# Performance work log

Hardware: AMD Instinct MI355X
Metric: run time of the kernel (lower is better)

The kernel has to match this reference:

```python
import jax, jax.numpy as jnp
import numpy as np

N = 16384   # flat token count
D = 256     # d_model
M = 64      # median_size (attention in_features / hidden_features)
OUT = 1     # output_size


def setup_inputs() -> dict:
    key = jax.random.key(0)
    ks = jax.random.split(key, 12)
    sD = 1.0 / np.sqrt(D)
    sM = 1.0 / np.sqrt(M)
    rn = lambda k, shape, s: (jax.random.normal(k, shape, jnp.float32) * s)
    return {
        "x":    rn(ks[0], (N, D), 1.0),
        "W1":   rn(ks[1], (D, M), sD), "b1": jnp.zeros((M,), jnp.float32),
        # 3 stacked attention blocks
        "Wq":   rn(ks[2], (3, M, M), sM), "bq": jnp.zeros((3, M), jnp.float32),
        "Wk":   rn(ks[3], (3, M, M), sM), "bk": jnp.zeros((3, M), jnp.float32),
        "Wv":   rn(ks[4], (3, M, M), sM), "bv": jnp.zeros((3, M), jnp.float32),
        "Wf1":  rn(ks[5], (3, M, M), sM), "bf1": jnp.zeros((3, M), jnp.float32),
        "Wf2":  rn(ks[6], (3, M, M), sM), "bf2": jnp.zeros((3, M), jnp.float32),
        "ln_g": jnp.ones((3, M), jnp.float32), "ln_b": jnp.zeros((3, M), jnp.float32),
        "Wout": rn(ks[7], (M, OUT), sM), "bout": jnp.zeros((OUT,), jnp.float32),
    }


def leaky(x, slope):
    return jnp.where(x >= 0, x, slope * x)


def layer_norm(x, g, b, eps=1e-5):
    mu = jnp.mean(x, axis=-1, keepdims=True)
    var = jnp.mean((x - mu) ** 2, axis=-1, keepdims=True)
    return (x - mu) * jax.lax.rsqrt(var + eps) * g + b


def attn_block(x, Wq, bq, Wk, bk, Wv, bv, Wf1, bf1, Wf2, bf2):
    # per-token outer-product attention: attn[n] = softmax(q[n] k[n]^T) over last dim
    q = x @ Wq + bq            # [N, M]
    k = x @ Wk + bk
    v = x @ Wv + bv
    a = jax.nn.softmax(q[:, :, None] * k[:, None, :], axis=-1)   # [N, M, M]
    y = jnp.einsum('nij,nj->ni', a, v) + x                       # residual add (x += x0)
    h = leaky(y @ Wf1 + bf1, 0.01)                               # LeakyReLU(0.01)
    h = h @ Wf2 + bf2
    return h + y                                                 # pred=False residual


def reference(x, W1, b1, Wq, bq, Wk, bk, Wv, bv, Wf1, bf1, Wf2, bf2, ln_g, ln_b, Wout, bout):
    h = x @ W1 + b1                 # Linear_1
    res = leaky(h, 0.1)             # x1 = LeakyReLU(0.1)(h)
    cur = h                         # transformer_1 is applied to pre-activation h
    for t in range(3):
        a = attn_block(cur, Wq[t], bq[t], Wk[t], bk[t], Wv[t], bv[t],
                       Wf1[t], bf1[t], Wf2[t], bf2[t])
        a = layer_norm(a, ln_g[t], ln_b[t])
        res = a + res               # x2 = LN(...) + x1, etc.
        cur = res
    out = leaky(res @ Wout + bout, 0.1).reshape(-1, OUT)
    return (out, out, out, out, out)
```

## Files before the change

kernel.cpp:

```cpp
#include <hip/hip_runtime.h>

#define NTOK 16384
#define TB 16

typedef float f32x4_t __attribute__((ext_vector_type(4)));
typedef short s16x8_t __attribute__((ext_vector_type(8)));
typedef short s16x4_t __attribute__((ext_vector_type(4)));

__device__ __forceinline__ unsigned short f2bf(float f) {
    unsigned int x = __float_as_uint(f);
    x += 0x7fffu + ((x >> 16) & 1u);
    return (unsigned short)(x >> 16);
}
__device__ __forceinline__ float fexp2(float x) {
#if __has_builtin(__builtin_amdgcn_exp2f)
    return __builtin_amdgcn_exp2f(x);
#else
    return exp2f(x);
#endif
}
__device__ __forceinline__ float frcp(float x) {
#if __has_builtin(__builtin_amdgcn_rcpf)
    return __builtin_amdgcn_rcpf(x);
#else
    return 1.0f / x;
#endif
}
__device__ __forceinline__ float frsq(float x) {
#if __has_builtin(__builtin_amdgcn_rsqf)
    return __builtin_amdgcn_rsqf(x);
#else
    return rsqrtf(x);
#endif
}

__global__ __launch_bounds__(256, 4)
void tf3_kernel(const float* __restrict__ x,
                const float* __restrict__ W1, const float* __restrict__ b1,
                const float* __restrict__ Wq, const float* __restrict__ bq,
                const float* __restrict__ Wk, const float* __restrict__ bk,
                const float* __restrict__ Wv, const float* __restrict__ bv,
                const float* __restrict__ Wf1, const float* __restrict__ bf1,
                const float* __restrict__ Wf2, const float* __restrict__ bf2,
                const float* __restrict__ lng, const float* __restrict__ lnb,
                const float* __restrict__ Wout, const float* __restrict__ bout,
                float* __restrict__ out)
{
    __shared__ __align__(16) unsigned short w3_lds[3 * 64 * 64];
    __shared__ __align__(16) unsigned short a_lds[TB * 64];
    __shared__ __align__(16) float q_lds[TB * 64];
    __shared__ __align__(16) float ky_lds[TB * 68];
    __shared__ __align__(16) float v_lds[TB * 64];

    const int tid = threadIdx.x;
    const int wv  = tid >> 6;
    const int l   = tid & 63;
    const int n0  = blockIdx.x * TB;

    const int lr  = l & 15;
    const int q4  = l >> 4;
    const int pcol = wv * 16;
    const int c    = pcol + lr;

    const int g  = q4;
    const int e  = lr;
    const int tg = wv * 4 + g;

    float res_reg[4], cur_reg[4];

    auto loadW = [&](const float* __restrict__ Wg, int slot, int cc) {
        s16x8_t pk;
        #pragma unroll
        for (int i = 0; i < 8; ++i)
            pk[i] = (short)f2bf(Wg[(cc * 8 + i) * 64 + l]);
        *reinterpret_cast<s16x8_t*>(&w3_lds[slot * 4096 + l * 64 + ((cc ^ (l & 7)) * 8)]) = pk;
    };
    auto mm16 = [&](const unsigned short* __restrict__ bbase) -> f32x4_t {
        f32x4_t acc = {0.f, 0.f, 0.f, 0.f};
        #pragma unroll
        for (int kh = 0; kh < 2; ++kh) {
            const int ck = kh * 4 + q4;
            const s16x8_t af = *reinterpret_cast<const s16x8_t*>(&a_lds[lr * 64 + ((ck ^ (lr & 7)) * 8)]);
            const s16x8_t bf = *reinterpret_cast<const s16x8_t*>(&bbase[c * 64 + ((ck ^ (c & 7)) * 8)]);
            acc = __builtin_amdgcn_mfma_f32_16x16x32_bf16(af, bf, acc, 0, 0, 0);
        }
        return acc;
    };

    f32x4_t acch = {0.f, 0.f, 0.f, 0.f};
    for (int kc = 0; kc < 4; ++kc) {
        __syncthreads();
        {
            const int r  = tid >> 4;
            const int c4 = (tid & 15) * 4;
            const float4 u = *reinterpret_cast<const float4*>(x + (size_t)(n0 + r) * 256 + kc * 64 + c4);
            s16x4_t pk;
            pk[0] = (short)f2bf(u.x); pk[1] = (short)f2bf(u.y);
            pk[2] = (short)f2bf(u.z); pk[3] = (short)f2bf(u.w);
            const int cc = c4 >> 3, e0 = c4 & 7;
            *reinterpret_cast<s16x4_t*>(&a_lds[r * 64 + ((cc ^ (r & 7)) * 8) + e0]) = pk;
        }
        loadW(W1 + kc * 4096, 0, wv * 2 + 0);
        loadW(W1 + kc * 4096, 0, wv * 2 + 1);
        __syncthreads();
        #pragma unroll
        for (int kh = 0; kh < 2; ++kh) {
            const int ck = kh * 4 + q4;
            const s16x8_t af = *reinterpret_cast<const s16x8_t*>(&a_lds[lr * 64 + ((ck ^ (lr & 7)) * 8)]);
            const s16x8_t bf = *reinterpret_cast<const s16x8_t*>(&w3_lds[c * 64 + ((ck ^ (c & 7)) * 8)]);
            acch = __builtin_amdgcn_mfma_f32_16x16x32_bf16(af, bf, acch, 0, 0, 0);
        }
    }
    {
        const float b1v = b1[c];
        #pragma unroll
        for (int rg = 0; rg < 4; ++rg)
            q_lds[(q4 * 4 + rg) * 64 + c] = acch[rg] + b1v;
    }
    __syncthreads();
    #pragma unroll
    for (int tt = 0; tt < 4; ++tt) {
        const int t = wv * 4 + tt;
        const float h = q_lds[t * 64 + l];
        cur_reg[tt] = h;
        res_reg[tt] = h >= 0.f ? h : 0.1f * h;
        a_lds[t * 64 + (((l >> 3) ^ (t & 7)) * 8) + (l & 7)] = f2bf(h);
    }

    for (int st = 0; st < 3; ++st) {
        const float* Wq_s  = Wq  + st * 4096;
        const float* Wk_s  = Wk  + st * 4096;
        const float* Wv_s  = Wv  + st * 4096;
        const float* Wf1_s = Wf1 + st * 4096;
        const float* Wf2_s = Wf2 + st * 4096;

        #pragma unroll
        for (int i = 0; i < 6; ++i) {
            const int u = wv * 6 + i;
            const int m = u >> 3;
            loadW(m == 0 ? Wq_s : (m == 1 ? Wk_s : Wv_s), m, u & 7);
        }
        __syncthreads();

        {
            f32x4_t aq = mm16(&w3_lds[0]);
            f32x4_t ak = mm16(&w3_lds[4096]);
            f32x4_t av = mm16(&w3_lds[8192]);
            const float bqv = bq[st * 64 + c];
            const float bkv = bk[st * 64 + c];
            const float bvv = bv[st * 64 + c];
            #pragma unroll
            for (int rg = 0; rg < 4; ++rg) {
                const int tr = q4 * 4 + rg;
                q_lds[tr * 64 + c]  = aq[rg] + bqv;
                ky_lds[tr * 68 + c] = ak[rg] + bkv;
                v_lds[tr * 64 + c]  = av[rg] + bvv;
            }
        }
        __syncthreads();

        #pragma unroll
        for (int i = 0; i < 4; ++i) {
            const int u = wv * 4 + i;
            loadW((u >> 3) == 0 ? Wf1_s : Wf2_s, u >> 3, u & 7);
        }
        float kmx, kmn;
        {
            const float4 kv = *reinterpret_cast<const float4*>(&ky_lds[tg * 68 + e * 4]);
            kmx = fmaxf(fmaxf(kv.x, kv.y), fmaxf(kv.z, kv.w));
            kmn = fminf(fminf(kv.x, kv.y), fminf(kv.z, kv.w));
            #pragma unroll
            for (int m = 1; m < 16; m <<= 1) {
                kmx = fmaxf(kmx, __shfl_xor(kmx, m, 64));
                kmn = fminf(kmn, __shfl_xor(kmn, m, 64));
            }
        }
        float kmax_t[4], kmin_t[4];
        #pragma unroll
        for (int tt = 0; tt < 4; ++tt) {
            kmax_t[tt] = __shfl(kmx, tt * 16, 64);
            kmin_t[tt] = __shfl(kmn, tt * 16, 64);
        }
        #pragma unroll
        for (int tt = 0; tt < 4; ++tt) {
            const int t = wv * 4 + tt;
            const float qs = q_lds[t * 64 + l] * 1.44269504088896340736f;
            const float m2 = fmaxf(qs * kmax_t[tt], qs * kmin_t[tt]);
            float s0 = 0.f, s1 = 0.f, p0 = 0.f, p1 = 0.f;
            #pragma unroll
            for (int j = 0; j < 64; j += 4) {
                const float4 kj = *reinterpret_cast<const float4*>(&ky_lds[t * 68 + j]);
                const float4 vj = *reinterpret_cast<const float4*>(&v_lds[t * 64 + j]);
                const float e0 = fexp2(fmaf(qs, kj.x, -m2));
                const float e1 = fexp2(fmaf(qs, kj.y, -m2));
                const float e2 = fexp2(fmaf(qs, kj.z, -m2));
                const float e3 = fexp2(fmaf(qs, kj.w, -m2));
                s0 += e0 + e2; s1 += e1 + e3;
                p0 = fmaf(e0, vj.x, p0); p1 = fmaf(e1, vj.y, p1);
                p0 = fmaf(e2, vj.z, p0); p1 = fmaf(e3, vj.w, p1);
            }
            const float y = (p0 + p1) * frcp(s0 + s1) + cur_reg[tt];
            ky_lds[t * 68 + l] = y;
        }
        __syncthreads();

        {
            f32x4_t acc = {0.f, 0.f, 0.f, 0.f};
            #pragma unroll
            for (int kh = 0; kh < 2; ++kh) {
                const float* yp = &ky_lds[lr * 68 + kh * 32 + q4 * 8];
                const float4 y0 = *reinterpret_cast<const float4*>(yp);
                const float4 y1 = *reinterpret_cast<const float4*>(yp + 4);
                s16x8_t af;
                af[0] = (short)f2bf(y0.x); af[1] = (short)f2bf(y0.y);
                af[2] = (short)f2bf(y0.z); af[3] = (short)f2bf(y0.w);
                af[4] = (short)f2bf(y1.x); af[5] = (short)f2bf(y1.y);
                af[6] = (short)f2bf(y1.z); af[7] = (short)f2bf(y1.w);
                const int ck = kh * 4 + q4;
                const s16x8_t bf = *reinterpret_cast<const s16x8_t*>(&w3_lds[c * 64 + ((ck ^ (c & 7)) * 8)]);
                acc = __builtin_amdgcn_mfma_f32_16x16x32_bf16(af, bf, acc, 0, 0, 0);
            }
            const float bfv = bf1[st * 64 + c];
            #pragma unroll
            for (int rg = 0; rg < 4; ++rg) {
                const int tr = q4 * 4 + rg;
                float h = acc[rg] + bfv;
                h = h >= 0.f ? h : 0.01f * h;
                a_lds[tr * 64 + (((c >> 3) ^ (tr & 7)) * 8) + (c & 7)] = f2bf(h);
            }
        }
        __syncthreads();

        {
            f32x4_t acc = mm16(&w3_lds[4096]);
            const float bfv = bf2[st * 64 + c];
            #pragma unroll
            for (int rg = 0; rg < 4; ++rg) {
                const int tr = q4 * 4 + rg;
                ky_lds[tr * 68 + c] += acc[rg] + bfv;
            }
        }
        __syncthreads();

        float s_sum, vsum;
        float4 av4;
        {
            av4 = *reinterpret_cast<const float4*>(&ky_lds[tg * 68 + e * 4]);
            s_sum = av4.x + av4.y + av4.z + av4.w;
            #pragma unroll
            for (int m = 1; m < 16; m <<= 1) s_sum += __shfl_xor(s_sum, m, 64);
            const float mug = s_sum * 0.015625f;
            const float d0 = av4.x - mug, d1 = av4.y - mug, d2 = av4.z - mug, d3 = av4.w - mug;
            vsum = d0 * d0 + d1 * d1 + d2 * d2 + d3 * d3;
            #pragma unroll
            for (int m = 1; m < 16; m <<= 1) vsum += __shfl_xor(vsum, m, 64);
            s_sum = mug;
        }
        const float lngv = lng[st * 64 + l];
        const float lnbv = lnb[st * 64 + l];
        #pragma unroll
        for (int tt = 0; tt < 4; ++tt) {
            const int t = wv * 4 + tt;
            const float mu = __shfl(s_sum, tt * 16, 64);
            const float vv = __shfl(vsum, tt * 16, 64);
            const float rs = frsq(vv * 0.015625f + 1e-5f);
            const float a  = ky_lds[t * 68 + l];
            const float an = (a - mu) * rs * lngv + lnbv;
            const float rnew = res_reg[tt] + an;
            res_reg[tt] = rnew;
            cur_reg[tt] = rnew;
            a_lds[t * 64 + (((l >> 3) ^ (t & 7)) * 8) + (l & 7)] = f2bf(rnew);
        }
    }

    const float wo = Wout[l];
    const float bo = bout[0];
    #pragma unroll
    for (int tt = 0; tt < 4; ++tt)
        q_lds[(wv * 4 + tt) * 64 + l] = res_reg[tt] * wo;
    {
        const float4 pv = *reinterpret_cast<const float4*>(&q_lds[tg * 64 + e * 4]);
        float p = pv.x + pv.y + pv.z + pv.w;
        #pragma unroll
        for (int m = 1; m < 16; m <<= 1) p += __shfl_xor(p, m, 64);
        if (e == 0) {
            float o = p + bo;
            o = o >= 0.f ? o : 0.1f * o;
            #pragma unroll
            for (int c5 = 0; c5 < 5; ++c5)
                out[(size_t)c5 * NTOK + n0 + tg] = o;
        }
    }
}

extern "C" void kernel_launch(void* const* d_in, const int* in_sizes, int n_in,
                              void* d_out, int out_size, void* d_ws, size_t ws_size,
                              hipStream_t stream) {
    const float* x    = (const float*)d_in[0];
    const float* W1   = (const float*)d_in[1];
    const float* b1   = (const float*)d_in[2];
    const float* Wq   = (const float*)d_in[3];
    const float* bq   = (const float*)d_in[4];
    const float* Wk   = (const float*)d_in[5];
    const float* bk   = (const float*)d_in[6];
    const float* Wv   = (const float*)d_in[7];
    const float* bv   = (const float*)d_in[8];
    const float* Wf1  = (const float*)d_in[9];
    const float* bf1  = (const float*)d_in[10];
    const float* Wf2  = (const float*)d_in[11];
    const float* bf2  = (const float*)d_in[12];
    const float* lngp = (const float*)d_in[13];
    const float* lnbp = (const float*)d_in[14];
    const float* Wout = (const float*)d_in[15];
    const float* bout = (const float*)d_in[16];
    float* outp = (float*)d_out;

    dim3 grid(NTOK / TB);
    dim3 block(256);
    hipLaunchKernelGGL(tf3_kernel, grid, block, 0, stream,
                       x, W1, b1, Wq, bq, Wk, bk, Wv, bv,
                       Wf1, bf1, Wf2, bf2, lngp, lnbp, Wout, bout, outp);
}
```

Measured before the change: 58.29 us.

## Pre-convert weights to bf16 once and read MFMA B-operands from global memory

```diff
diff --git a/kernel.cpp b/kernel.cpp
--- a/kernel.cpp
+++ b/kernel.cpp
@@ -1,11 +1,10 @@
 #include <hip/hip_runtime.h>
 
 #define NTOK 16384
-#define TB 16
+#define TB 8
 
 typedef float f32x4_t __attribute__((ext_vector_type(4)));
 typedef short s16x8_t __attribute__((ext_vector_type(8)));
-typedef short s16x4_t __attribute__((ext_vector_type(4)));
 
 __device__ __forceinline__ unsigned short f2bf(float f) {
     unsigned int x = __float_as_uint(f);
@@ -34,23 +33,42 @@
 #endif
 }
 
-__global__ __launch_bounds__(256, 4)
+__global__ __launch_bounds__(256)
+void prep_kernel(const float* __restrict__ W1,
+                 const float* __restrict__ Wq, const float* __restrict__ Wk,
+                 const float* __restrict__ Wv, const float* __restrict__ Wf1,
+                 const float* __restrict__ Wf2, unsigned short* __restrict__ wsb)
+{
+    const int i = blockIdx.x * 256 + threadIdx.x;
+    if (i < 16384) {
+        const int m = i >> 8, k = i & 255;
+        wsb[i] = f2bf(W1[k * 64 + m]);
+    } else if (i < 77824) {
+        const int u  = i - 16384;
+        const int mm = u >> 12;
+        const int st = mm / 5, q = mm % 5;
+        const int r  = u & 4095;
+        const int m  = r >> 6, k = r & 63;
+        const float* src = q == 0 ? Wq : q == 1 ? Wk : q == 2 ? Wv : q == 3 ? Wf1 : Wf2;
+        wsb[i] = f2bf(src[st * 4096 + k * 64 + m]);
+    }
+}
+
+__global__ __launch_bounds__(256, 8)
 void tf3_kernel(const float* __restrict__ x,
-                const float* __restrict__ W1, const float* __restrict__ b1,
-                const float* __restrict__ Wq, const float* __restrict__ bq,
-                const float* __restrict__ Wk, const float* __restrict__ bk,
-                const float* __restrict__ Wv, const float* __restrict__ bv,
-                const float* __restrict__ Wf1, const float* __restrict__ bf1,
-                const float* __restrict__ Wf2, const float* __restrict__ bf2,
+                const float* __restrict__ b1,
+                const float* __restrict__ bq, const float* __restrict__ bk,
+                const float* __restrict__ bv,
+                const float* __restrict__ bf1, const float* __restrict__ bf2,
                 const float* __restrict__ lng, const float* __restrict__ lnb,
                 const float* __restrict__ Wout, const float* __restrict__ bout,
+                const unsigned short* __restrict__ wsb,
                 float* __restrict__ out)
 {
-    __shared__ __align__(16) unsigned short w3_lds[3 * 64 * 64];
-    __shared__ __align__(16) unsigned short a_lds[TB * 64];
-    __shared__ __align__(16) float q_lds[TB * 64];
-    __shared__ __align__(16) float ky_lds[TB * 68];
-    __shared__ __align__(16) float v_lds[TB * 64];
+    __shared__ __align__(16) unsigned short a_lds[16 * 64];
+    __shared__ __align__(16) float q_lds[16 * 68];
+    __shared__ __align__(16) float ky_lds[16 * 68];
+    __shared__ __align__(16) float v_lds[16 * 68];
 
     const int tid = threadIdx.x;
     const int wv  = tid >> 6;
@@ -59,145 +77,113 @@
 
     const int lr  = l & 15;
     const int q4  = l >> 4;
-    const int pcol = wv * 16;
-    const int c    = pcol + lr;
-
-    const int g  = q4;
-    const int e  = lr;
-    const int tg = wv * 4 + g;
-
-    float res_reg[4], cur_reg[4];
-
-    auto loadW = [&](const float* __restrict__ Wg, int slot, int cc) {
-        s16x8_t pk;
+    const int c   = wv * 16 + lr;
+
+    const int hh = l >> 5;
+    const int e2 = l & 31;
+    const int th = wv * 2 + hh;
+
+    float res_reg[2], cur_reg[2];
+
+    {
+        const float* xrow = x + (size_t)min(n0 + lr, NTOK - 1) * 256;
+        f32x4_t acch = {0.f, 0.f, 0.f, 0.f};
         #pragma unroll
-        for (int i = 0; i < 8; ++i)
-            pk[i] = (short)f2bf(Wg[(cc * 8 + i) * 64 + l]);
-        *reinterpret_cast<s16x8_t*>(&w3_lds[slot * 4096 + l * 64 + ((cc ^ (l & 7)) * 8)]) = pk;
-    };
-    auto mm16 = [&](const unsigned short* __restrict__ bbase) -> f32x4_t {
-        f32x4_t acc = {0.f, 0.f, 0.f, 0.f};
-        #pragma unroll
-        for (int kh = 0; kh < 2; ++kh) {
-            const int ck = kh * 4 + q4;
-            const s16x8_t af = *reinterpret_cast<const s16x8_t*>(&a_lds[lr * 64 + ((ck ^ (lr & 7)) * 8)]);
-            const s16x8_t bf = *reinterpret_cast<const s16x8_t*>(&bbase[c * 64 + ((ck ^ (c & 7)) * 8)]);
-            acc = __builtin_amdgcn_mfma_f32_16x16x32_bf16(af, bf, acc, 0, 0, 0);
-        }
-        return acc;
-    };
-
-    f32x4_t acch = {0.f, 0.f, 0.f, 0.f};
-    for (int kc = 0; kc < 4; ++kc) {
-        __syncthreads();
-        {
-            const int r  = tid >> 4;
-            const int c4 = (tid & 15) * 4;
-            const float4 u = *reinterpret_cast<const float4*>(x + (size_t)(n0 + r) * 256 + kc * 64 + c4);
-            s16x4_t pk;
-            pk[0] = (short)f2bf(u.x); pk[1] = (short)f2bf(u.y);
-            pk[2] = (short)f2bf(u.z); pk[3] = (short)f2bf(u.w);
-            const int cc = c4 >> 3, e0 = c4 & 7;
-            *reinterpret_cast<s16x4_t*>(&a_lds[r * 64 + ((cc ^ (r & 7)) * 8) + e0]) = pk;
-        }
-        loadW(W1 + kc * 4096, 0, wv * 2 + 0);
-        loadW(W1 + kc * 4096, 0, wv * 2 + 1);
-        __syncthreads();
-        #pragma unroll
-        for (int kh = 0; kh < 2; ++kh) {
-            const int ck = kh * 4 + q4;
-            const s16x8_t af = *reinterpret_cast<const s16x8_t*>(&a_lds[lr * 64 + ((ck ^ (lr & 7)) * 8)]);
-            const s16x8_t bf = *reinterpret_cast<const s16x8_t*>(&w3_lds[c * 64 + ((ck ^ (c & 7)) * 8)]);
+        for (int s5 = 0; s5 < 8; ++s5) {
+            const int k0 = s5 * 32 + q4 * 8;
+            const float4 u0 = *reinterpret_cast<const float4*>(xrow + k0);
+            const float4 u1 = *reinterpret_cast<const float4*>(xrow + k0 + 4);
+            s16x8_t af;
+            af[0] = (short)f2bf(u0.x); af[1] = (short)f2bf(u0.y);
+            af[2] = (short)f2bf(u0.z); af[3] = (short)f2bf(u0.w);
+            af[4] = (short)f2bf(u1.x); af[5] = (short)f2bf(u1.y);
+            af[6] = (short)f2bf(u1.z); af[7] = (short)f2bf(u1.w);
+            const s16x8_t bf = *reinterpret_cast<const s16x8_t*>(&wsb[c * 256 + k0]);
             acch = __builtin_amdgcn_mfma_f32_16x16x32_bf16(af, bf, acch, 0, 0, 0);
         }
-    }
-    {
-        const float b1v = b1[c];
+        const float bb = b1[c];
         #pragma unroll
         for (int rg = 0; rg < 4; ++rg)
-            q_lds[(q4 * 4 + rg) * 64 + c] = acch[rg] + b1v;
+            q_lds[(q4 * 4 + rg) * 68 + c] = acch[rg] + bb;
     }
     __syncthreads();
     #pragma unroll
-    for (int tt = 0; tt < 4; ++tt) {
-        const int t = wv * 4 + tt;
-        const float h = q_lds[t * 64 + l];
+    for (int tt = 0; tt < 2; ++tt) {
+        const int t = wv * 2 + tt;
+        const float h = q_lds[t * 68 + l];
         cur_reg[tt] = h;
         res_reg[tt] = h >= 0.f ? h : 0.1f * h;
         a_lds[t * 64 + (((l >> 3) ^ (t & 7)) * 8) + (l & 7)] = f2bf(h);
     }
 
     for (int st = 0; st < 3; ++st) {
-        const float* Wq_s  = Wq  + st * 4096;
-        const float* Wk_s  = Wk  + st * 4096;
-        const float* Wv_s  = Wv  + st * 4096;
-        const float* Wf1_s = Wf1 + st * 4096;
-        const float* Wf2_s = Wf2 + st * 4096;
-
-        #pragma unroll
-        for (int i = 0; i < 6; ++i) {
-            const int u = wv * 6 + i;
-            const int m = u >> 3;
-            loadW(m == 0 ? Wq_s : (m == 1 ? Wk_s : Wv_s), m, u & 7);
-        }
-        __syncthreads();
-
-        {
-            f32x4_t aq = mm16(&w3_lds[0]);
-            f32x4_t ak = mm16(&w3_lds[4096]);
-            f32x4_t av = mm16(&w3_lds[8192]);
-            const float bqv = bq[st * 64 + c];
-            const float bkv = bk[st * 64 + c];
-            const float bvv = bv[st * 64 + c];
-            #pragma unroll
-            for (int rg = 0; rg < 4; ++rg) {
-                const int tr = q4 * 4 + rg;
-                q_lds[tr * 64 + c]  = aq[rg] + bqv;
-                ky_lds[tr * 68 + c] = ak[rg] + bkv;
-                v_lds[tr * 64 + c]  = av[rg] + bvv;
-            }
-        }
-        __syncthreads();
-
-        #pragma unroll
-        for (int i = 0; i < 4; ++i) {
-            const int u = wv * 4 + i;
-            loadW((u >> 3) == 0 ? Wf1_s : Wf2_s, u >> 3, u & 7);
-        }
-        float kmx, kmn;
-        {
-            const float4 kv = *reinterpret_cast<const float4*>(&ky_lds[tg * 68 + e * 4]);
-            kmx = fmaxf(fmaxf(kv.x, kv.y), fmaxf(kv.z, kv.w));
-            kmn = fminf(fminf(kv.x, kv.y), fminf(kv.z, kv.w));
-            #pragma unroll
-            for (int m = 1; m < 16; m <<= 1) {
+        const unsigned short* WS = wsb + 16384 + st * 5 * 4096;
+
+        __syncthreads();
+        const s16x8_t af0 = *reinterpret_cast<const s16x8_t*>(&a_lds[lr * 64 + ((q4       ^ (lr & 7)) * 8)]);
+        const s16x8_t af1 = *reinterpret_cast<const s16x8_t*>(&a_lds[lr * 64 + (((4 + q4) ^ (lr & 7)) * 8)]);
+        {
+            const s16x8_t b0 = *reinterpret_cast<const s16x8_t*>(&WS[c * 64 + q4 * 8]);
+            const s16x8_t b1f = *reinterpret_cast<const s16x8_t*>(&WS[c * 64 + 32 + q4 * 8]);
+            f32x4_t acc = __builtin_amdgcn_mfma_f32_16x16x32_bf16(af0, b0, (f32x4_t){0.f,0.f,0.f,0.f}, 0, 0, 0);
+            acc = __builtin_amdgcn_mfma_f32_16x16x32_bf16(af1, b1f, acc, 0, 0, 0);
+            const float bb = bq[st * 64 + c];
+            #pragma unroll
+            for (int rg = 0; rg < 4; ++rg) q_lds[(q4 * 4 + rg) * 68 + c] = acc[rg] + bb;
+        }
+        {
+            const s16x8_t b0 = *reinterpret_cast<const s16x8_t*>(&WS[4096 + c * 64 + q4 * 8]);
+            const s16x8_t b1f = *reinterpret_cast<const s16x8_t*>(&WS[4096 + c * 64 + 32 + q4 * 8]);
+            f32x4_t acc = __builtin_amdgcn_mfma_f32_16x16x32_bf16(af0, b0, (f32x4_t){0.f,0.f,0.f,0.f}, 0, 0, 0);
+            acc = __builtin_amdgcn_mfma_f32_16x16x32_bf16(af1, b1f, acc, 0, 0, 0);
+            const float bb = bk[st * 64 + c];
+            #pragma unroll
+            for (int rg = 0; rg < 4; ++rg) ky_lds[(q4 * 4 + rg) * 68 + c] = acc[rg] + bb;
+        }
+        {
+            const s16x8_t b0 = *reinterpret_cast<const s16x8_t*>(&WS[8192 + c * 64 + q4 * 8]);
+            const s16x8_t b1f = *reinterpret_cast<const s16x8_t*>(&WS[8192 + c * 64 + 32 + q4 * 8]);
+            f32x4_t acc = __builtin_amdgcn_mfma_f32_16x16x32_bf16(af0, b0, (f32x4_t){0.f,0.f,0.f,0.f}, 0, 0, 0);
+            acc = __builtin_amdgcn_mfma_f32_16x16x32_bf16(af1, b1f, acc, 0, 0, 0);
+            const float bb = bv[st * 64 + c];
+            #pragma unroll
+            for (int rg = 0; rg < 4; ++rg) v_lds[(q4 * 4 + rg) * 68 + c] = acc[rg] + bb;
+        }
+        __syncthreads();
+
+        float kmax_t[2], kmin_t[2];
+        {
+            const float2 kv = *reinterpret_cast<const float2*>(&ky_lds[th * 68 + e2 * 2]);
+            float kmx = fmaxf(kv.x, kv.y);
+            float kmn = fminf(kv.x, kv.y);
+            #pragma unroll
+            for (int m = 1; m < 32; m <<= 1) {
                 kmx = fmaxf(kmx, __shfl_xor(kmx, m, 64));
                 kmn = fminf(kmn, __shfl_xor(kmn, m, 64));
             }
-        }
-        float kmax_t[4], kmin_t[4];
+            #pragma unroll
+            for (int tt = 0; tt < 2; ++tt) {
+                kmax_t[tt] = __shfl(kmx, tt * 32, 64);
+                kmin_t[tt] = __shfl(kmn, tt * 32, 64);
+            }
+        }
         #pragma unroll
-        for (int tt = 0; tt < 4; ++tt) {
-            kmax_t[tt] = __shfl(kmx, tt * 16, 64);
-            kmin_t[tt] = __shfl(kmn, tt * 16, 64);
-        }
-        #pragma unroll
-        for (int tt = 0; tt < 4; ++tt) {
-            const int t = wv * 4 + tt;
-            const float qs = q_lds[t * 64 + l] * 1.44269504088896340736f;
+        for (int tt = 0; tt < 2; ++tt) {
+            const int t = wv * 2 + tt;
+            const float qs = q_lds[t * 68 + l] * 1.44269504088896340736f;
             const float m2 = fmaxf(qs * kmax_t[tt], qs * kmin_t[tt]);
             float s0 = 0.f, s1 = 0.f, p0 = 0.f, p1 = 0.f;
             #pragma unroll
             for (int j = 0; j < 64; j += 4) {
                 const float4 kj = *reinterpret_cast<const float4*>(&ky_lds[t * 68 + j]);
-                const float4 vj = *reinterpret_cast<const float4*>(&v_lds[t * 64 + j]);
+                const float4 vj = *reinterpret_cast<const float4*>(&v_lds[t * 68 + j]);
                 const float e0 = fexp2(fmaf(qs, kj.x, -m2));
                 const float e1 = fexp2(fmaf(qs, kj.y, -m2));
-                const float e2 = fexp2(fmaf(qs, kj.z, -m2));
+                const float e2v = fexp2(fmaf(qs, kj.z, -m2));
                 const float e3 = fexp2(fmaf(qs, kj.w, -m2));
-                s0 += e0 + e2; s1 += e1 + e3;
+                s0 += e0 + e2v; s1 += e1 + e3;
                 p0 = fmaf(e0, vj.x, p0); p1 = fmaf(e1, vj.y, p1);
-                p0 = fmaf(e2, vj.z, p0); p1 = fmaf(e3, vj.w, p1);
+                p0 = fmaf(e2v, vj.z, p0); p1 = fmaf(e3, vj.w, p1);
             }
             const float y = (p0 + p1) * frcp(s0 + s1) + cur_reg[tt];
             ky_lds[t * 68 + l] = y;
@@ -216,15 +202,14 @@
                 af[2] = (short)f2bf(y0.z); af[3] = (short)f2bf(y0.w);
                 af[4] = (short)f2bf(y1.x); af[5] = (short)f2bf(y1.y);
                 af[6] = (short)f2bf(y1.z); af[7] = (short)f2bf(y1.w);
-                const int ck = kh * 4 + q4;
-                const s16x8_t bf = *reinterpret_cast<const s16x8_t*>(&w3_lds[c * 64 + ((ck ^ (c & 7)) * 8)]);
+                const s16x8_t bf = *reinterpret_cast<const s16x8_t*>(&WS[3 * 4096 + c * 64 + kh * 32 + q4 * 8]);
                 acc = __builtin_amdgcn_mfma_f32_16x16x32_bf16(af, bf, acc, 0, 0, 0);
             }
-            const float bfv = bf1[st * 64 + c];
+            const float bb = bf1[st * 64 + c];
             #pragma unroll
             for (int rg = 0; rg < 4; ++rg) {
                 const int tr = q4 * 4 + rg;
-                float h = acc[rg] + bfv;
+                float h = acc[rg] + bb;
                 h = h >= 0.f ? h : 0.01f * h;
                 a_lds[tr * 64 + (((c >> 3) ^ (tr & 7)) * 8) + (c & 7)] = f2bf(h);
             }
@@ -232,63 +217,65 @@
         __syncthreads();
 
         {
-            f32x4_t acc = mm16(&w3_lds[4096]);
-            const float bfv = bf2[st * 64 + c];
+            const s16x8_t ag0 = *reinterpret_cast<const s16x8_t*>(&a_lds[lr * 64 + ((q4       ^ (lr & 7)) * 8)]);
+            const s16x8_t ag1 = *reinterpret_cast<const s16x8_t*>(&a_lds[lr * 64 + (((4 + q4) ^ (lr & 7)) * 8)]);
+            const s16x8_t b0 = *reinterpret_cast<const s16x8_t*>(&WS[4 * 4096 + c * 64 + q4 * 8]);
+            const s16x8_t b1f = *reinterpret_cast<const s16x8_t*>(&WS[4 * 4096 + c * 64 + 32 + q4 * 8]);
+            f32x4_t acc = __builtin_amdgcn_mfma_f32_16x16x32_bf16(ag0, b0, (f32x4_t){0.f,0.f,0.f,0.f}, 0, 0, 0);
+            acc = __builtin_amdgcn_mfma_f32_16x16x32_bf16(ag1, b1f, acc, 0, 0, 0);
+            const float bb = bf2[st * 64 + c];
             #pragma unroll
             for (int rg = 0; rg < 4; ++rg) {
                 const int tr = q4 * 4 + rg;
-                ky_lds[tr * 68 + c] += acc[rg] + bfv;
-            }
-        }
-        __syncthreads();
-
-        float s_sum, vsum;
-        float4 av4;
-        {
-            av4 = *reinterpret_cast<const float4*>(&ky_lds[tg * 68 + e * 4]);
-            s_sum = av4.x + av4.y + av4.z + av4.w;
-            #pragma unroll
-            for (int m = 1; m < 16; m <<= 1) s_sum += __shfl_xor(s_sum, m, 64);
-            const float mug = s_sum * 0.015625f;
-            const float d0 = av4.x - mug, d1 = av4.y - mug, d2 = av4.z - mug, d3 = av4.w - mug;
-            vsum = d0 * d0 + d1 * d1 + d2 * d2 + d3 * d3;
-            #pragma unroll
-            for (int m = 1; m < 16; m <<= 1) vsum += __shfl_xor(vsum, m, 64);
-            s_sum = mug;
-        }
-        const float lngv = lng[st * 64 + l];
-        const float lnbv = lnb[st * 64 + l];
-        #pragma unroll
-        for (int tt = 0; tt < 4; ++tt) {
-            const int t = wv * 4 + tt;
-            const float mu = __shfl(s_sum, tt * 16, 64);
-            const float vv = __shfl(vsum, tt * 16, 64);
-            const float rs = frsq(vv * 0.015625f + 1e-5f);
-            const float a  = ky_lds[t * 68 + l];
-            const float an = (a - mu) * rs * lngv + lnbv;
-            const float rnew = res_reg[tt] + an;
-            res_reg[tt] = rnew;
-            cur_reg[tt] = rnew;
-            a_lds[t * 64 + (((l >> 3) ^ (t & 7)) * 8) + (l & 7)] = f2bf(rnew);
+                ky_lds[tr * 68 + c] += acc[rg] + bb;
+            }
+        }
+        __syncthreads();
+
+        {
+            const float2 av2 = *reinterpret_cast<const float2*>(&ky_lds[th * 68 + e2 * 2]);
+            float ssum = av2.x + av2.y;
+            #pragma unroll
+            for (int m = 1; m < 32; m <<= 1) ssum += __shfl_xor(ssum, m, 64);
+            const float mug = ssum * 0.015625f;
+            const float d0 = av2.x - mug, d1 = av2.y - mug;
+            float vsum = d0 * d0 + d1 * d1;
+            #pragma unroll
+            for (int m = 1; m < 32; m <<= 1) vsum += __shfl_xor(vsum, m, 64);
+            const float lngv = lng[st * 64 + l];
+            const float lnbv = lnb[st * 64 + l];
+            #pragma unroll
+            for (int tt = 0; tt < 2; ++tt) {
+                const int t = wv * 2 + tt;
+                const float mu = __shfl(mug, tt * 32, 64);
+                const float vv = __shfl(vsum, tt * 32, 64);
+                const float rs = frsq(vv * 0.015625f + 1e-5f);
+                const float a  = ky_lds[t * 68 + l];
+                const float an = (a - mu) * rs * lngv + lnbv;
+                const float rnew = res_reg[tt] + an;
+                res_reg[tt] = rnew;
+                cur_reg[tt] = rnew;
+                a_lds[t * 64 + (((l >> 3) ^ (t & 7)) * 8) + (l & 7)] = f2bf(rnew);
+            }
         }
     }
 
     const float wo = Wout[l];
     const float bo = bout[0];
     #pragma unroll
-    for (int tt = 0; tt < 4; ++tt)
-        q_lds[(wv * 4 + tt) * 64 + l] = res_reg[tt] * wo;
+    for (int tt = 0; tt < 2; ++tt)
+        q_lds[(wv * 2 + tt) * 68 + l] = res_reg[tt] * wo;
     {
-        const float4 pv = *reinterpret_cast<const float4*>(&q_lds[tg * 64 + e * 4]);
-        float p = pv.x + pv.y + pv.z + pv.w;
+        const float2 pv = *reinterpret_cast<const float2*>(&q_lds[th * 68 + e2 * 2]);
+        float p = pv.x + pv.y;
         #pragma unroll
-        for (int m = 1; m < 16; m <<= 1) p += __shfl_xor(p, m, 64);
-        if (e == 0) {
+        for (int m = 1; m < 32; m <<= 1) p += __shfl_xor(p, m, 64);
+        if (e2 == 0) {
             float o = p + bo;
             o = o >= 0.f ? o : 0.1f * o;
             #pragma unroll
             for (int c5 = 0; c5 < 5; ++c5)
-                out[(size_t)c5 * NTOK + n0 + tg] = o;
+                out[(size_t)c5 * NTOK + n0 + th] = o;
         }
     }
 }
@@ -314,10 +301,11 @@
     const float* Wout = (const float*)d_in[15];
     const float* bout = (const float*)d_in[16];
     float* outp = (float*)d_out;
-
-    dim3 grid(NTOK / TB);
-    dim3 block(256);
-    hipLaunchKernelGGL(tf3_kernel, grid, block, 0, stream,
-                       x, W1, b1, Wq, bq, Wk, bk, Wv, bv,
-                       Wf1, bf1, Wf2, bf2, lngp, lnbp, Wout, bout, outp);
-}
+    unsigned short* wsb = (unsigned short*)d_ws;
+
+    hipLaunchKernelGGL(prep_kernel, dim3(304), dim3(256), 0, stream,
+                       W1, Wq, Wk, Wv, Wf1, Wf2, wsb);
+    hipLaunchKernelGGL(tf3_kernel, dim3(NTOK / TB), dim3(256), 0, stream,
+                       x, b1, bq, bk, bv, bf1, bf2, lngp, lnbp, Wout, bout,
+                       (const unsigned short*)wsb, outp);
+}
```

After: 110.9 us. +90.3%, slower.
